# Performance work log

Hardware: AMD Instinct MI355X
Metric: run time of the kernel (lower is better)

The kernel has to match this reference:

```python
import jax, jax.numpy as jnp
import numpy as np

NP = 16   # attention heads
HN = 128  # head dim (kv_channels)
MASK_VAL = -10000.0  # attention_mask_func fill value in TE


def setup_inputs() -> dict:
    key = jax.random.key(0)
    ks = jax.random.split(key, 5)
    S, B, H = 2048, 1, 2048
    return {
        "hidden_states": jax.random.normal(ks[0], (S, B, H), jnp.float32),
        "w_qkv": jax.random.normal(ks[1], (3 * H, H), jnp.float32) * 0.02,
        "b_qkv": jax.random.normal(ks[2], (3 * H,), jnp.float32) * 0.02,
        "w_proj": jax.random.normal(ks[3], (H, H), jnp.float32) * 0.02,
        "b_proj": jax.random.normal(ks[4], (H,), jnp.float32) * 0.02,
        "attention_mask": jnp.zeros((1, 1, S, S), dtype=bool),
    }


def reference(hidden_states, w_qkv, b_qkv, w_proj, b_proj, attention_mask):
    S, B, H = hidden_states.shape
    # fused QKV GEMM: [s, b, 3h]
    qkv = jnp.einsum("sbh,oh->sbo", hidden_states, w_qkv) + b_qkv
    qkv = qkv.reshape(S, B, NP, 3 * HN)
    q, k, v = jnp.split(qkv, 3, axis=-1)  # each [s, b, np, hn]

    # BMM1: full [b, np, sq, sk] score matrix (naive unfused attention)
    norm_factor = jnp.asarray(np.sqrt(HN), q.dtype)
    scores = jnp.einsum("sbnh,tbnh->bnst", q, k) / norm_factor

    # causal mask (attn_mask_type='causal'); provided mask OR'd in (zeros here)
    causal = jnp.triu(jnp.ones((S, S), dtype=bool), 1)
    mask = jnp.logical_or(causal, attention_mask[0, 0])
    scores = jnp.where(mask, jnp.asarray(MASK_VAL, scores.dtype), scores)

    # softmax in fp32 (apply_query_key_layer_scaling forces fp32 softmax)
    probs = jax.nn.softmax(scores.astype(jnp.float32), axis=-1).astype(q.dtype)
    # dropout p=0.0 -> identity

    # BMM2 + merge heads -> [s, b, h]
    ctx = jnp.einsum("bnst,tbnh->sbnh", probs, v).reshape(S, B, H)

    # output projection (bias returned separately, return_bias=True)
    out = jnp.einsum("sbh,oh->sbo", ctx, w_proj)
    return out, b_proj
```

## Files before the change

kernel.cpp:

```cpp
#include <hip/hip_runtime.h>
#include <math.h>

#define S_LEN   2048
#define H_DIM   2048
#define QKV_LD  6144
#define N_HEADS 16
#define HEAD_DIM 128

typedef __attribute__((ext_vector_type(8))) short short8;
typedef __attribute__((ext_vector_type(4))) float f32x4;
typedef unsigned short ushort_t;

__device__ __forceinline__ ushort_t f2bf(float x) {
    unsigned int u = __float_as_uint(x);
    u = (u + 0x7fffu + ((u >> 16) & 1u)) >> 16;
    return (ushort_t)u;
}

#define GLOBAL_LOAD_LDS16(gp, lp)                                              \
    __builtin_amdgcn_global_load_lds(                                          \
        (const __attribute__((address_space(1))) void*)(gp),                   \
        (__attribute__((address_space(3))) void*)(lp), 16, 0, 0)

__global__ __launch_bounds__(256) void cvt_bf16(const float* __restrict__ src,
                                                ushort_t* __restrict__ dst) {
    const int i = (blockIdx.x * 256 + threadIdx.x) * 8;
    float4 a = *(const float4*)(src + i);
    float4 b = *(const float4*)(src + i + 4);
    short8 v;
    v[0] = f2bf(a.x); v[1] = f2bf(a.y); v[2] = f2bf(a.z); v[3] = f2bf(a.w);
    v[4] = f2bf(b.x); v[5] = f2bf(b.y); v[6] = f2bf(b.z); v[7] = f2bf(b.w);
    *(short8*)(dst + i) = v;
}

template <bool BIAS, bool OUT_BF16>
__global__ __launch_bounds__(256)
void gemm_bf16_nt(const ushort_t* __restrict__ A, const ushort_t* __restrict__ B,
                  const float* __restrict__ bias, void* __restrict__ Cout,
                  int M, int N, int K) {
    __shared__ __align__(16) ushort_t As[128 * 64];
    __shared__ __align__(16) ushort_t Bs[128 * 64];

    const int tid  = threadIdx.x;
    const int lane = tid & 63;
    const int w    = tid >> 6;
    const int wr   = w >> 1, wc = w & 1;
    const int m0   = blockIdx.y << 7;
    const int n0   = blockIdx.x << 7;
    const int frow = lane & 15;
    const int fk16 = (lane >> 4) << 4;

    f32x4 acc[4][4];
    #pragma unroll
    for (int i = 0; i < 4; i++)
        #pragma unroll
        for (int j = 0; j < 4; j++) acc[i][j] = (f32x4){0.f, 0.f, 0.f, 0.f};

    for (int k0 = 0; k0 < K; k0 += 64) {
        __syncthreads();
        #pragma unroll
        for (int i = 0; i < 4; i++) {
            const int off = (i * 256 + tid) * 8;
            const int r   = off >> 6;
            const int cb  = ((off & 63) * 2) ^ ((r & 7) << 4);
            GLOBAL_LOAD_LDS16((const char*)(A + (size_t)(m0 + r) * K + k0) + cb,
                              (char*)As + off * 2);
            GLOBAL_LOAD_LDS16((const char*)(B + (size_t)(n0 + r) * K + k0) + cb,
                              (char*)Bs + off * 2);
        }
        __syncthreads();
        #pragma unroll
        for (int kk = 0; kk < 2; kk++) {
            short8 a[4], b[4];
            #pragma unroll
            for (int mi = 0; mi < 4; mi++) {
                const int row = wr * 64 + mi * 16 + frow;
                const int cb  = (kk * 64 + fk16) ^ ((row & 7) << 4);
                a[mi] = *(const short8*)((const char*)As + row * 128 + cb);
            }
            #pragma unroll
            for (int ni = 0; ni < 4; ni++) {
                const int row = wc * 64 + ni * 16 + frow;
                const int cb  = (kk * 64 + fk16) ^ ((row & 7) << 4);
                b[ni] = *(const short8*)((const char*)Bs + row * 128 + cb);
            }
            #pragma unroll
            for (int mi = 0; mi < 4; mi++)
                #pragma unroll
                for (int ni = 0; ni < 4; ni++)
                    acc[mi][ni] = __builtin_amdgcn_mfma_f32_16x16x32_bf16(
                        a[mi], b[ni], acc[mi][ni], 0, 0, 0);
        }
    }

    const int crow0 = (lane >> 4) * 4;
    const int ccol  = lane & 15;
    #pragma unroll
    for (int mi = 0; mi < 4; mi++) {
        #pragma unroll
        for (int ni = 0; ni < 4; ni++) {
            const int col = n0 + wc * 64 + ni * 16 + ccol;
            const float bv = BIAS ? bias[col] : 0.f;
            #pragma unroll
            for (int r = 0; r < 4; r++) {
                const int row = m0 + wr * 64 + mi * 16 + crow0 + r;
                const float v = acc[mi][ni][r] + bv;
                if (OUT_BF16)
                    ((ushort_t*)Cout)[(size_t)row * N + col] = f2bf(v);
                else
                    ((float*)Cout)[(size_t)row * N + col] = v;
            }
        }
    }
}

__global__ __launch_bounds__(256)
void attn_mfma(const ushort_t* __restrict__ qkv, ushort_t* __restrict__ ctx) {
    __shared__ __align__(16) ushort_t Ks[64 * 136];
    __shared__ __align__(16) ushort_t Vt[128 * 72];
    __shared__ __align__(16) ushort_t Pl[4][16 * 72];

    const int tid  = threadIdx.x;
    const int lane = tid & 63;
    const int w    = tid >> 6;
    const int head = blockIdx.y;
    const int q0   = blockIdx.x << 6;
    const int frow = lane & 15;
    const int fhi  = lane >> 4;
    const size_t hbase = (size_t)head * 384;
    ushort_t* plw = &Pl[w][0];

    short8 aq[4];
    {
        const ushort_t* qrow = qkv + (size_t)(q0 + w * 16 + frow) * QKV_LD + hbase;
        #pragma unroll
        for (int ks = 0; ks < 4; ks++)
            aq[ks] = *(const short8*)(qrow + ks * 32 + fhi * 8);
    }

    f32x4 acc[8];
    #pragma unroll
    for (int nd = 0; nd < 8; nd++) acc[nd] = (f32x4){0.f, 0.f, 0.f, 0.f};
    float m_run[4], l_run[4];
    #pragma unroll
    for (int r = 0; r < 4; r++) { m_run[r] = -INFINITY; l_run[r] = 0.f; }

    const int ntiles = (q0 >> 6) + 1;
    for (int kt = 0; kt < ntiles; kt++) {
        const int k0 = kt << 6;
        __syncthreads();
        #pragma unroll
        for (int i = 0; i < 4; i++) {
            const int c = i * 256 + tid;
            const int key = c >> 4, ch = c & 15;
            short8 kv = *(const short8*)(qkv + (size_t)(k0 + key) * QKV_LD + hbase + 128 + ch * 8);
            *(short8*)(Ks + key * 136 + ch * 8) = kv;
        }
        #pragma unroll
        for (int i = 0; i < 4; i++) {
            const int c = i * 256 + tid;
            const int key = c & 63, dc = c >> 6;
            short8 vv = *(const short8*)(qkv + (size_t)(k0 + key) * QKV_LD + hbase + 256 + dc * 8);
            #pragma unroll
            for (int j = 0; j < 8; j++) Vt[(dc * 8 + j) * 72 + key] = vv[j];
        }
        __syncthreads();

        f32x4 s[4];
        #pragma unroll
        for (int ni = 0; ni < 4; ni++) s[ni] = (f32x4){0.f, 0.f, 0.f, 0.f};
        #pragma unroll
        for (int ks = 0; ks < 4; ks++) {
            #pragma unroll
            for (int ni = 0; ni < 4; ni++) {
                short8 bk = *(const short8*)(Ks + (ni * 16 + frow) * 136 + ks * 32 + fhi * 8);
                s[ni] = __builtin_amdgcn_mfma_f32_16x16x32_bf16(aq[ks], bk, s[ni], 0, 0, 0);
            }
        }

        const float norm = 0.08838834764831843f;
        const bool last = (kt == ntiles - 1);
        #pragma unroll
        for (int ni = 0; ni < 4; ni++)
            #pragma unroll
            for (int r = 0; r < 4; r++) {
                float v = s[ni][r] * norm;
                if (last && (k0 + ni * 16 + frow > q0 + w * 16 + fhi * 4 + r))
                    v = -INFINITY;
                s[ni][r] = v;
            }

        float mnew[4];
        #pragma unroll
        for (int r = 0; r < 4; r++) {
            float t = fmaxf(fmaxf(s[0][r], s[1][r]), fmaxf(s[2][r], s[3][r]));
            t = fmaxf(t, __shfl_xor(t, 1));
            t = fmaxf(t, __shfl_xor(t, 2));
            t = fmaxf(t, __shfl_xor(t, 4));
            t = fmaxf(t, __shfl_xor(t, 8));
            mnew[r] = fmaxf(m_run[r], t);
        }
        float psum[4] = {0.f, 0.f, 0.f, 0.f};
        #pragma unroll
        for (int ni = 0; ni < 4; ni++)
            #pragma unroll
            for (int r = 0; r < 4; r++) {
                const float p = __expf(s[ni][r] - mnew[r]);
                psum[r] += p;
                plw[(fhi * 4 + r) * 72 + ni * 16 + frow] = f2bf(p);
            }
        #pragma unroll
        for (int r = 0; r < 4; r++) {
            float t = psum[r];
            t += __shfl_xor(t, 1); t += __shfl_xor(t, 2);
            t += __shfl_xor(t, 4); t += __shfl_xor(t, 8);
            const float sc = __expf(m_run[r] - mnew[r]);
            l_run[r] = l_run[r] * sc + t;
            m_run[r] = mnew[r];
            #pragma unroll
            for (int nd = 0; nd < 8; nd++) acc[nd][r] *= sc;
        }

        #pragma unroll
        for (int ks = 0; ks < 2; ks++) {
            short8 ap = *(const short8*)(plw + frow * 72 + ks * 32 + fhi * 8);
            #pragma unroll
            for (int nd = 0; nd < 8; nd++) {
                short8 bv = *(const short8*)(Vt + (nd * 16 + frow) * 72 + ks * 32 + fhi * 8);
                acc[nd] = __builtin_amdgcn_mfma_f32_16x16x32_bf16(ap, bv, acc[nd], 0, 0, 0);
            }
        }
    }

    #pragma unroll
    for (int r = 0; r < 4; r++) {
        const float inv = 1.f / l_run[r];
        const int row = q0 + w * 16 + fhi * 4 + r;
        #pragma unroll
        for (int nd = 0; nd < 8; nd++)
            ctx[(size_t)row * H_DIM + head * HEAD_DIM + nd * 16 + frow] =
                f2bf(acc[nd][r] * inv);
    }
}

__global__ __launch_bounds__(256) void copy_bias(const float* __restrict__ b,
                                                 float* __restrict__ out) {
    const int i = blockIdx.x * 256 + threadIdx.x;
    if (i < H_DIM) out[i] = b[i];
}

extern "C" void kernel_launch(void* const* d_in, const int* in_sizes, int n_in,
                              void* d_out, int out_size, void* d_ws, size_t ws_size,
                              hipStream_t stream) {
    const float* hidden = (const float*)d_in[0];
    const float* w_qkv  = (const float*)d_in[1];
    const float* b_qkv  = (const float*)d_in[2];
    const float* w_proj = (const float*)d_in[3];
    const float* b_proj = (const float*)d_in[4];
    float* out = (float*)d_out;

    ushort_t* qkvb = (ushort_t*)d_ws;
    ushort_t* bufB = qkvb + (size_t)S_LEN * QKV_LD;
    ushort_t* bufC = bufB + (size_t)S_LEN * H_DIM;

    cvt_bf16<<<dim3((S_LEN * H_DIM) / 2048), 256, 0, stream>>>(hidden, bufB);
    cvt_bf16<<<dim3((QKV_LD * H_DIM) / 2048), 256, 0, stream>>>(w_qkv, bufC);

    gemm_bf16_nt<true, true><<<dim3(QKV_LD / 128, S_LEN / 128), 256, 0, stream>>>(
        bufB, bufC, b_qkv, qkvb, S_LEN, QKV_LD, H_DIM);

    cvt_bf16<<<dim3((H_DIM * H_DIM) / 2048), 256, 0, stream>>>(w_proj, bufC);

    attn_mfma<<<dim3(S_LEN / 64, N_HEADS), 256, 0, stream>>>(qkvb, bufB);

    gemm_bf16_nt<false, false><<<dim3(H_DIM / 128, S_LEN / 128), 256, 0, stream>>>(
        bufB, bufC, nullptr, out, S_LEN, H_DIM, H_DIM);

    copy_bias<<<dim3((H_DIM + 255) / 256), 256, 0, stream>>>(
        b_proj, out + (size_t)S_LEN * H_DIM);
}
```

Before: 407.8 us.

## Rewrite causal attention with 32x32 MFMA, double-buffered K/V and balanced tiles

Replaces the attention kernel with a 128-thread version. It computes S^T using 32x32x16 MFMAs and keeps P in registers through cvt_pk plus permlane32 swaps instead of routing it through LDS. K is staged with swizzled direct global-to-LDS loads and V is transposed into double-buffered LDS, so the next tile's loads overlap current compute. Each block handles a low and a high query tile pair to balance the causal workload. The cost is a grid of only 256 blocks, which may leave CUs idle, plus higher register pressure.

```diff
diff --git a/kernel.cpp b/kernel.cpp
--- a/kernel.cpp
+++ b/kernel.cpp
@@ -9,6 +9,7 @@
 
 typedef __attribute__((ext_vector_type(8))) short short8;
 typedef __attribute__((ext_vector_type(4))) float f32x4;
+typedef __attribute__((ext_vector_type(16))) float f32x16;
 typedef unsigned short ushort_t;
 
 __device__ __forceinline__ ushort_t f2bf(float x) {
@@ -17,10 +18,32 @@
     return (ushort_t)u;
 }
 
+__device__ __forceinline__ unsigned cvtpk_bf16(float a, float b) {
+    unsigned r;
+    asm("v_cvt_pk_bf16_f32 %0, %1, %2" : "=v"(r) : "v"(a), "v"(b));
+    return r;
+}
+
+__device__ __forceinline__ void plswap(unsigned &a, unsigned &b) {
+    typedef unsigned uv2 __attribute__((ext_vector_type(2)));
+    uv2 r = __builtin_amdgcn_permlane32_swap(a, b, false, false);
+    a = r[0]; b = r[1];
+}
+
 #define GLOBAL_LOAD_LDS16(gp, lp)                                              \
     __builtin_amdgcn_global_load_lds(                                          \
         (const __attribute__((address_space(1))) void*)(gp),                   \
         (__attribute__((address_space(3))) void*)(lp), 16, 0, 0)
+
+#define MKFRAG(P, base, out) {                                                 \
+    unsigned wa = cvtpk_bf16(P[(base)+0], P[(base)+1]);                        \
+    unsigned wb = cvtpk_bf16(P[(base)+4], P[(base)+5]);                        \
+    unsigned wc = cvtpk_bf16(P[(base)+2], P[(base)+3]);                        \
+    unsigned wd = cvtpk_bf16(P[(base)+6], P[(base)+7]);                        \
+    plswap(wa, wb); plswap(wc, wd);                                            \
+    union { unsigned u[4]; short8 s; } fu;                                     \
+    fu.u[0] = wa; fu.u[1] = wc; fu.u[2] = wb; fu.u[3] = wd;                    \
+    out = fu.s; }
 
 __global__ __launch_bounds__(256) void cvt_bf16(const float* __restrict__ src,
                                                 ushort_t* __restrict__ dst) {
@@ -114,132 +137,179 @@
     }
 }
 
-__global__ __launch_bounds__(256)
-void attn_mfma(const ushort_t* __restrict__ qkv, ushort_t* __restrict__ ctx) {
-    __shared__ __align__(16) ushort_t Ks[64 * 136];
-    __shared__ __align__(16) ushort_t Vt[128 * 72];
-    __shared__ __align__(16) ushort_t Pl[4][16 * 72];
+__global__ __launch_bounds__(128)
+void attn_mfma2(const ushort_t* __restrict__ qkv, ushort_t* __restrict__ ctx)
+{
+    __shared__ __align__(16) ushort_t Ks[2][64 * 128];
+    __shared__ __align__(16) ushort_t Vt[2][128 * 72];
 
     const int tid  = threadIdx.x;
     const int lane = tid & 63;
     const int w    = tid >> 6;
+    const int b    = blockIdx.x;
     const int head = blockIdx.y;
-    const int q0   = blockIdx.x << 6;
-    const int frow = lane & 15;
-    const int fhi  = lane >> 4;
+    const int l31  = lane & 31;
+    const int hi   = lane >> 5;
     const size_t hbase = (size_t)head * 384;
-    ushort_t* plw = &Pl[w][0];
-
-    short8 aq[4];
-    {
-        const ushort_t* qrow = qkv + (size_t)(q0 + w * 16 + frow) * QKV_LD + hbase;
-        #pragma unroll
-        for (int ks = 0; ks < 4; ks++)
-            aq[ks] = *(const short8*)(qrow + ks * 32 + fhi * 8);
-    }
-
-    f32x4 acc[8];
-    #pragma unroll
-    for (int nd = 0; nd < 8; nd++) acc[nd] = (f32x4){0.f, 0.f, 0.f, 0.f};
-    float m_run[4], l_run[4];
-    #pragma unroll
-    for (int r = 0; r < 4; r++) { m_run[r] = -INFINITY; l_run[r] = 0.f; }
-
-    const int ntiles = (q0 >> 6) + 1;
-    for (int kt = 0; kt < ntiles; kt++) {
+    const ushort_t* kbase = qkv + hbase + 128;
+    const ushort_t* vbase = qkv + hbase + 256;
+    const int kq = tid & 15;
+    const int dc = tid >> 4;
+
+    short8 vreg[8];
+
+    auto stage_k = [&](int kt, ushort_t* dst) {
+        const int krow0 = kt << 6;
+        #pragma unroll
+        for (int i = 0; i < 8; i++) {
+            const int off  = (i * 128 + tid) * 8;
+            const int r    = off >> 7;
+            const int slot = (off & 127) >> 3;
+            const int sb   = (slot ^ (r & 15)) << 4;
+            GLOBAL_LOAD_LDS16(
+                (const char*)(kbase + (size_t)(krow0 + r) * QKV_LD) + sb,
+                (char*)dst + off * 2);
+        }
+    };
+    auto load_v = [&](int kt) {
         const int k0 = kt << 6;
+        #pragma unroll
+        for (int kk = 0; kk < 4; kk++)
+            #pragma unroll
+            for (int h2 = 0; h2 < 2; h2++)
+                vreg[kk * 2 + h2] = *(const short8*)(vbase +
+                    (size_t)(k0 + 4 * kq + kk) * QKV_LD + dc * 16 + h2 * 8);
+    };
+    auto write_vt = [&](ushort_t* dst) {
+        #pragma unroll
+        for (int j = 0; j < 16; j++) {
+            const int h2 = j >> 3, e = j & 7;
+            unsigned lo = (unsigned)(unsigned short)vreg[0 + h2][e] |
+                          ((unsigned)(unsigned short)vreg[2 + h2][e] << 16);
+            unsigned hh = (unsigned)(unsigned short)vreg[4 + h2][e] |
+                          ((unsigned)(unsigned short)vreg[6 + h2][e] << 16);
+            unsigned long long v64 =
+                (unsigned long long)lo | ((unsigned long long)hh << 32);
+            *(unsigned long long*)(dst + (dc * 16 + j) * 72 + 4 * kq) = v64;
+        }
+    };
+
+    #pragma unroll 1
+    for (int phase = 0; phase < 2; phase++) {
+        const int qt = (phase == 0) ? (2 * b + w) : (63 - 2 * b - w);
+        const int nt = (phase == 0) ? (b + 1) : (32 - b);
+        const int q  = qt * 32 + l31;
+
+        short8 qf[8];
+        const ushort_t* qrow = qkv + (size_t)q * QKV_LD + hbase;
+        #pragma unroll
+        for (int ks = 0; ks < 8; ks++)
+            qf[ks] = *(const short8*)(qrow + ks * 16 + hi * 8);
+
+        f32x16 accO[4];
+        #pragma unroll
+        for (int dt = 0; dt < 4; dt++)
+            #pragma unroll
+            for (int i = 0; i < 16; i++) accO[dt][i] = 0.f;
+        float m_run = -INFINITY, l_run = 0.f;
+
+        stage_k(0, Ks[0]);
+        load_v(0);
         __syncthreads();
-        #pragma unroll
-        for (int i = 0; i < 4; i++) {
-            const int c = i * 256 + tid;
-            const int key = c >> 4, ch = c & 15;
-            short8 kv = *(const short8*)(qkv + (size_t)(k0 + key) * QKV_LD + hbase + 128 + ch * 8);
-            *(short8*)(Ks + key * 136 + ch * 8) = kv;
-        }
-        #pragma unroll
-        for (int i = 0; i < 4; i++) {
-            const int c = i * 256 + tid;
-            const int key = c & 63, dc = c >> 6;
-            short8 vv = *(const short8*)(qkv + (size_t)(k0 + key) * QKV_LD + hbase + 256 + dc * 8);
-            #pragma unroll
-            for (int j = 0; j < 8; j++) Vt[(dc * 8 + j) * 72 + key] = vv[j];
-        }
+        write_vt(Vt[0]);
         __syncthreads();
 
-        f32x4 s[4];
-        #pragma unroll
-        for (int ni = 0; ni < 4; ni++) s[ni] = (f32x4){0.f, 0.f, 0.f, 0.f};
-        #pragma unroll
-        for (int ks = 0; ks < 4; ks++) {
-            #pragma unroll
-            for (int ni = 0; ni < 4; ni++) {
-                short8 bk = *(const short8*)(Ks + (ni * 16 + frow) * 136 + ks * 32 + fhi * 8);
-                s[ni] = __builtin_amdgcn_mfma_f32_16x16x32_bf16(aq[ks], bk, s[ni], 0, 0, 0);
-            }
-        }
-
-        const float norm = 0.08838834764831843f;
-        const bool last = (kt == ntiles - 1);
-        #pragma unroll
-        for (int ni = 0; ni < 4; ni++)
-            #pragma unroll
-            for (int r = 0; r < 4; r++) {
-                float v = s[ni][r] * norm;
-                if (last && (k0 + ni * 16 + frow > q0 + w * 16 + fhi * 4 + r))
-                    v = -INFINITY;
-                s[ni][r] = v;
-            }
-
-        float mnew[4];
-        #pragma unroll
-        for (int r = 0; r < 4; r++) {
-            float t = fmaxf(fmaxf(s[0][r], s[1][r]), fmaxf(s[2][r], s[3][r]));
-            t = fmaxf(t, __shfl_xor(t, 1));
-            t = fmaxf(t, __shfl_xor(t, 2));
-            t = fmaxf(t, __shfl_xor(t, 4));
-            t = fmaxf(t, __shfl_xor(t, 8));
-            mnew[r] = fmaxf(m_run[r], t);
-        }
-        float psum[4] = {0.f, 0.f, 0.f, 0.f};
-        #pragma unroll
-        for (int ni = 0; ni < 4; ni++)
-            #pragma unroll
-            for (int r = 0; r < 4; r++) {
-                const float p = __expf(s[ni][r] - mnew[r]);
-                psum[r] += p;
-                plw[(fhi * 4 + r) * 72 + ni * 16 + frow] = f2bf(p);
-            }
-        #pragma unroll
-        for (int r = 0; r < 4; r++) {
-            float t = psum[r];
-            t += __shfl_xor(t, 1); t += __shfl_xor(t, 2);
-            t += __shfl_xor(t, 4); t += __shfl_xor(t, 8);
-            const float sc = __expf(m_run[r] - mnew[r]);
-            l_run[r] = l_run[r] * sc + t;
-            m_run[r] = mnew[r];
-            #pragma unroll
-            for (int nd = 0; nd < 8; nd++) acc[nd][r] *= sc;
-        }
-
-        #pragma unroll
-        for (int ks = 0; ks < 2; ks++) {
-            short8 ap = *(const short8*)(plw + frow * 72 + ks * 32 + fhi * 8);
-            #pragma unroll
-            for (int nd = 0; nd < 8; nd++) {
-                short8 bv = *(const short8*)(Vt + (nd * 16 + frow) * 72 + ks * 32 + fhi * 8);
-                acc[nd] = __builtin_amdgcn_mfma_f32_16x16x32_bf16(ap, bv, acc[nd], 0, 0, 0);
-            }
-        }
-    }
-
-    #pragma unroll
-    for (int r = 0; r < 4; r++) {
-        const float inv = 1.f / l_run[r];
-        const int row = q0 + w * 16 + fhi * 4 + r;
-        #pragma unroll
-        for (int nd = 0; nd < 8; nd++)
-            ctx[(size_t)row * H_DIM + head * HEAD_DIM + nd * 16 + frow] =
-                f2bf(acc[nd][r] * inv);
+        for (int kt = 0; kt < nt; kt++) {
+            const int cur = kt & 1;
+            const ushort_t* Kc = Ks[cur];
+            const ushort_t* Vc = Vt[cur];
+            const bool pre = (kt + 1 < nt);
+            if (pre) { stage_k(kt + 1, Ks[cur ^ 1]); load_v(kt + 1); }
+
+            f32x16 s0, s1;
+            #pragma unroll
+            for (int i = 0; i < 16; i++) { s0[i] = 0.f; s1[i] = 0.f; }
+            __builtin_amdgcn_s_setprio(1);
+            #pragma unroll
+            for (int ks = 0; ks < 8; ks++) {
+                const int sb = (((2 * ks + hi) ^ (l31 & 15)) << 4);
+                short8 kf0 = *(const short8*)((const char*)Kc + l31 * 256 + sb);
+                short8 kf1 = *(const short8*)((const char*)Kc + (32 + l31) * 256 + sb);
+                s0 = __builtin_amdgcn_mfma_f32_32x32x16_bf16(kf0, qf[ks], s0, 0, 0, 0);
+                s1 = __builtin_amdgcn_mfma_f32_32x32x16_bf16(kf1, qf[ks], s1, 0, 0, 0);
+            }
+            __builtin_amdgcn_s_setprio(0);
+
+            const float norm = 0.08838834764831843f;
+            const int k0g = kt * 64;
+            float p0[16], p1[16];
+            #pragma unroll
+            for (int r = 0; r < 16; r++) {
+                const int kp = (r & 3) + 8 * (r >> 2) + 4 * hi;
+                float v0 = s0[r] * norm;
+                float v1 = s1[r] * norm;
+                if (kt == nt - 1) {
+                    if (k0g + kp > q)      v0 = -INFINITY;
+                    if (k0g + 32 + kp > q) v1 = -INFINITY;
+                }
+                p0[r] = v0; p1[r] = v1;
+            }
+            float mx = fmaxf(p0[0], p1[0]);
+            #pragma unroll
+            for (int r = 1; r < 16; r++) mx = fmaxf(mx, fmaxf(p0[r], p1[r]));
+            mx = fmaxf(mx, __shfl_xor(mx, 32));
+            const float mnew = fmaxf(m_run, mx);
+            float ps = 0.f;
+            #pragma unroll
+            for (int r = 0; r < 16; r++) {
+                p0[r] = __expf(p0[r] - mnew);
+                p1[r] = __expf(p1[r] - mnew);
+                ps += p0[r] + p1[r];
+            }
+            ps += __shfl_xor(ps, 32);
+            const float sc = __expf(m_run - mnew);
+            l_run = l_run * sc + ps;
+            m_run = mnew;
+            #pragma unroll
+            for (int dt = 0; dt < 4; dt++)
+                #pragma unroll
+                for (int i = 0; i < 16; i++) accO[dt][i] *= sc;
+
+            short8 pf[4];
+            MKFRAG(p0, 0, pf[0]); MKFRAG(p0, 8, pf[1]);
+            MKFRAG(p1, 0, pf[2]); MKFRAG(p1, 8, pf[3]);
+
+            if (pre) write_vt(Vt[cur ^ 1]);
+
+            __builtin_amdgcn_s_setprio(1);
+            #pragma unroll
+            for (int dt = 0; dt < 4; dt++)
+                #pragma unroll
+                for (int ks = 0; ks < 4; ks++) {
+                    short8 vf = *(const short8*)(Vc + (dt * 32 + l31) * 72 +
+                                                 ks * 16 + hi * 8);
+                    accO[dt] = __builtin_amdgcn_mfma_f32_32x32x16_bf16(
+                        vf, pf[ks], accO[dt], 0, 0, 0);
+                }
+            __builtin_amdgcn_s_setprio(0);
+            __syncthreads();
+        }
+
+        const float inv = 1.f / l_run;
+        ushort_t* crow = ctx + (size_t)q * H_DIM + head * HEAD_DIM;
+        #pragma unroll
+        for (int dblk = 0; dblk < 8; dblk++) {
+            const int dt = dblk >> 1;
+            const int base = (dblk & 1) * 8;
+            unsigned wa = cvtpk_bf16(accO[dt][base + 0] * inv, accO[dt][base + 1] * inv);
+            unsigned wb = cvtpk_bf16(accO[dt][base + 4] * inv, accO[dt][base + 5] * inv);
+            unsigned wc = cvtpk_bf16(accO[dt][base + 2] * inv, accO[dt][base + 3] * inv);
+            unsigned wd = cvtpk_bf16(accO[dt][base + 6] * inv, accO[dt][base + 7] * inv);
+            plswap(wa, wb); plswap(wc, wd);
+            union { unsigned u[4]; short8 s; } fu;
+            fu.u[0] = wa; fu.u[1] = wc; fu.u[2] = wb; fu.u[3] = wd;
+            *(short8*)(crow + dblk * 16 + hi * 8) = fu.s;
+        }
     }
 }
 
@@ -271,7 +341,7 @@
 
     cvt_bf16<<<dim3((H_DIM * H_DIM) / 2048), 256, 0, stream>>>(w_proj, bufC);
 
-    attn_mfma<<<dim3(S_LEN / 64, N_HEADS), 256, 0, stream>>>(qkvb, bufB);
+    attn_mfma2<<<dim3(16, N_HEADS), 128, 0, stream>>>(qkvb, bufB);
 
     gemm_bf16_nt<false, false><<<dim3(H_DIM / 128, S_LEN / 128), 256, 0, stream>>>(
         bufB, bufC, nullptr, out, S_LEN, H_DIM, H_DIM);
```

New measurement: 356.2 us. 1.14x faster.
